# Kernel optimization log

Measured on AMD Instinct MI355X. Metric: run time of the kernel, lower is better.

## Reference

```python
import jax, jax.numpy as jnp
import numpy as np
from jax import lax

N, M, B = 512, 1024, 1024  # signal dim, atoms, batch (batch==m required by X = W @ Gamma)
POWER_ITER = 100
IHT_ITER = 50


def setup_inputs() -> dict:
    key = jax.random.key(0)
    k1, k2 = jax.random.split(key)
    Y = jax.random.normal(k1, (B, N), dtype=jnp.float32)
    W = jax.random.normal(k2, (N, M), dtype=jnp.float32)
    return {"Y": Y, "W": W, "K": 64}


def power_method(W):
    # 100 iterations of X <- X W^T W / ||.||; returns last pre-normalization norm
    # (approx largest eigenvalue of W^T W), matching PowerMethod in the source.
    X0 = jax.random.normal(jax.random.key(42), (1, W.shape[1]), dtype=W.dtype)

    def body(i, carry):
        X, _ = carry
        X2 = (X @ W.T) @ W          # [1, m]
        nm = jnp.linalg.norm(X2)
        return (X2 / nm, nm)

    _, nm = lax.fori_loop(0, POWER_ITER, body, (X0, jnp.asarray(1.0, W.dtype)))
    return nm


def hard_threshold_k(G, K):
    # keep entries strictly larger (in abs) than the (K+1)-th largest per row
    a = jnp.sort(jnp.abs(G), axis=1)[:, ::-1]   # descending per row
    T = a[:, K][:, None]                          # [B, 1]
    return G * (jnp.abs(G) > T).astype(G.dtype)


def reference(Y, W, K):
    # NormDict: column-normalize the dictionary
    W = W / jnp.linalg.norm(W, axis=0)
    c = power_method(W)
    eta = 1.0 / c
    Yn = jnp.linalg.norm(Y)

    # IHT sparse coding
    Gamma = hard_threshold_k(Y @ (eta * W), K)     # [B, m]
    residual = Gamma @ W.T - Y                      # [B, n]

    def step(carry, _):
        Gamma, residual = carry
        Gamma = hard_threshold_k(Gamma - eta * (residual @ W), K)
        residual = Gamma @ W.T - Y
        return (Gamma, residual), jnp.linalg.norm(residual) / Yn

    (Gamma, residual), norms = lax.scan(step, (Gamma, residual), None, length=IHT_ITER)

    X = W @ Gamma  # [n, m] @ [B, m] -> requires B == m, as in the torch source
    return X, Gamma, norms
```

## Files before the change

kernel.cpp:

```cpp
#include <hip/hip_runtime.h>


#define DEV __device__ __forceinline__

constexpr int Nd = 512;
constexpr int Md = 1024;
constexpr int Bd = 1024;
constexpr int Ksp = 64;
constexpr int IHT = 50;

DEV float wave_reduce_f(float v) {
#pragma unroll
  for (int off = 32; off > 0; off >>= 1) v += __shfl_down(v, off);
  return v;
}
DEV double wave_reduce_d(double v) {
#pragma unroll
  for (int off = 32; off > 0; off >>= 1) v += __shfl_down(v, off);
  return v;
}

__global__ void k_zero(double* dacc) {
  int t = threadIdx.x;
  if (t < 51) dacc[t] = 0.0;
}

__global__ __launch_bounds__(256) void k_colnorm(const float* __restrict__ W,
                                                 float* __restrict__ cnorm) {
  int col = blockIdx.x * 256 + threadIdx.x;
  double ss = 0.0;
  for (int i = 0; i < Nd; ++i) {
    float w = W[(size_t)i * Md + col];
    ss = fma((double)w, (double)w, ss);
  }
  cnorm[col] = (float)sqrt(ss);
}

__global__ __launch_bounds__(256) void k_normalize(const float* __restrict__ W,
                                                   const float* __restrict__ cnorm,
                                                   float* __restrict__ Wn) {
  int idx = blockIdx.x * 256 + threadIdx.x;
  Wn[idx] = W[idx] / cnorm[idx & (Md - 1)];
}

__global__ __launch_bounds__(256) void k_yn2(const float* __restrict__ Y,
                                             double* __restrict__ dacc) {
  double s = 0.0;
  for (int i = blockIdx.x * 256 + threadIdx.x; i < Bd * Nd; i += gridDim.x * 256) {
    float y = Y[i];
    s = fma((double)y, (double)y, s);
  }
  s = wave_reduce_d(s);
  __shared__ double red[4];
  int lane = threadIdx.x & 63, wid = threadIdx.x >> 6;
  if (lane == 0) red[wid] = s;
  __syncthreads();
  if (threadIdx.x == 0) atomicAdd(&dacc[0], red[0] + red[1] + red[2] + red[3]);
}

template <int BM, int BN, int TN>
__global__ __launch_bounds__(256) void k_gemm_t(const float* __restrict__ A, int lda, int ta,
                                                const float* __restrict__ B, int ldb, int tb,
                                                float* __restrict__ C, int ldc, int Kd,
                                                float scale) {
  constexpr int AE = 32 * BM / 256;
  constexpr int BE = 32 * BN / 256;
  __shared__ __align__(16) float As[32][BM + 4];
  __shared__ __align__(16) float Bs[32][BN + 4];
  const int tid = threadIdx.x;
  const int tx = tid % (BN / TN), ty = tid / (BN / TN);
  const int m0 = blockIdx.y * BM, n0 = blockIdx.x * BN;
  float ra[AE], rb[BE];
  float acc[4][TN];
#pragma unroll
  for (int i = 0; i < 4; ++i)
#pragma unroll
    for (int j = 0; j < TN; ++j) acc[i][j] = 0.f;

  auto loadA = [&](int k0) {
    if (!ta) {
      const int c = tid & 31, r0 = tid >> 5;
#pragma unroll
      for (int i = 0; i < AE; ++i)
        ra[i] = A[(size_t)(m0 + r0 + i * 8) * lda + (k0 + c)];
    } else {
      const int r = tid % BM, c0 = tid / BM;
#pragma unroll
      for (int i = 0; i < AE; ++i)
        ra[i] = A[(size_t)(k0 + c0 + i * (256 / BM)) * lda + (m0 + r)];
    }
  };
  auto storeA = [&]() {
    if (!ta) {
      const int c = tid & 31, r0 = tid >> 5;
#pragma unroll
      for (int i = 0; i < AE; ++i) As[c][r0 + i * 8] = ra[i];
    } else {
      const int r = tid % BM, c0 = tid / BM;
#pragma unroll
      for (int i = 0; i < AE; ++i) As[c0 + i * (256 / BM)][r] = ra[i];
    }
  };
  auto loadB = [&](int k0) {
    if (!tb) {
      const int c = tid % BN, r0 = tid / BN;
#pragma unroll
      for (int i = 0; i < BE; ++i)
        rb[i] = B[(size_t)(k0 + r0 + i * (256 / BN)) * ldb + (n0 + c)];
    } else {
      const int r = tid & 31, c0 = tid >> 5;
#pragma unroll
      for (int i = 0; i < BE; ++i)
        rb[i] = B[(size_t)(n0 + c0 + i * 8) * ldb + (k0 + r)];
    }
  };
  auto storeB = [&]() {
    if (!tb) {
      const int c = tid % BN, r0 = tid / BN;
#pragma unroll
      for (int i = 0; i < BE; ++i) Bs[r0 + i * (256 / BN)][c] = rb[i];
    } else {
      const int r = tid & 31, c0 = tid >> 5;
#pragma unroll
      for (int i = 0; i < BE; ++i) Bs[r][c0 + i * 8] = rb[i];
    }
  };

  loadA(0);
  loadB(0);
  storeA();
  storeB();
  __syncthreads();
  for (int k0 = 0; k0 < Kd; k0 += 32) {
    const bool more = (k0 + 32) < Kd;
    if (more) { loadA(k0 + 32); loadB(k0 + 32); }
#pragma unroll
    for (int kk = 0; kk < 32; ++kk) {
      const float4 a4 = *(const float4*)&As[kk][ty * 4];
      const float aa[4] = {a4.x, a4.y, a4.z, a4.w};
      float bb[TN];
      if constexpr (TN == 4) {
        const float4 b4 = *(const float4*)&Bs[kk][tx * 4];
        bb[0] = b4.x; bb[1] = b4.y; bb[2] = b4.z; bb[3] = b4.w;
      } else {
        const float2 b2 = *(const float2*)&Bs[kk][tx * 2];
        bb[0] = b2.x; bb[1] = b2.y;
      }
#pragma unroll
      for (int i = 0; i < 4; ++i)
#pragma unroll
        for (int j = 0; j < TN; ++j) acc[i][j] = fmaf(aa[i], bb[j], acc[i][j]);
    }
    if (more) {
      __syncthreads();
      storeA();
      storeB();
      __syncthreads();
    }
  }
#pragma unroll
  for (int i = 0; i < 4; ++i) {
    if constexpr (TN == 4) {
      float4 o;
      o.x = acc[i][0] * scale; o.y = acc[i][1] * scale;
      o.z = acc[i][2] * scale; o.w = acc[i][3] * scale;
      *(float4*)&C[(size_t)(m0 + ty * 4 + i) * ldc + n0 + tx * 4] = o;
    } else {
      float2 o;
      o.x = acc[i][0] * scale; o.y = acc[i][1] * scale;
      *(float2*)&C[(size_t)(m0 + ty * 4 + i) * ldc + n0 + tx * 2] = o;
    }
  }
}

DEV float erfinv_xla(float x) {
  float w = -log1pf(-x * x);
  float p;
  if (w < 5.0f) {
    w = w - 2.5f;
    p = 2.81022636e-08f;
    p = fmaf(p, w, 3.43273939e-07f);
    p = fmaf(p, w, -3.5233877e-06f);
    p = fmaf(p, w, -4.39150654e-06f);
    p = fmaf(p, w, 0.00021858087f);
    p = fmaf(p, w, -0.00125372503f);
    p = fmaf(p, w, -0.00417768164f);
    p = fmaf(p, w, 0.246640727f);
    p = fmaf(p, w, 1.50140941f);
  } else {
    w = sqrtf(w) - 3.0f;
    p = -0.000200214257f;
    p = fmaf(p, w, 0.000100950558f);
    p = fmaf(p, w, 0.00134934322f);
    p = fmaf(p, w, -0.00367342844f);
    p = fmaf(p, w, 0.00573950773f);
    p = fmaf(p, w, -0.0076224613f);
    p = fmaf(p, w, 0.00943887047f);
    p = fmaf(p, w, 1.00167406f);
    p = fmaf(p, w, 2.83297682f);
  }
  return p * x;
}

#define TF_ROUND(r)                                  \
  {                                                  \
    x0 += x1;                                        \
    x1 = (x1 << (r)) | (x1 >> (32 - (r)));           \
    x1 ^= x0;                                        \
  }

__global__ void k_x0(float* __restrict__ X0) {
  unsigned i = threadIdx.x;
  unsigned x0 = i, x1 = i + 512u;
  const unsigned ks0 = 0u, ks1 = 42u, ks2 = 0x1BD11BDAu ^ 42u;
  x0 += ks0; x1 += ks1;
  TF_ROUND(13) TF_ROUND(15) TF_ROUND(26) TF_ROUND(6)  x0 += ks1; x1 += ks2 + 1u;
  TF_ROUND(17) TF_ROUND(29) TF_ROUND(16) TF_ROUND(24) x0 += ks2; x1 += ks0 + 2u;
  TF_ROUND(13) TF_ROUND(15) TF_ROUND(26) TF_ROUND(6)  x0 += ks0; x1 += ks1 + 3u;
  TF_ROUND(17) TF_ROUND(29) TF_ROUND(16) TF_ROUND(24) x0 += ks1; x1 += ks2 + 4u;
  TF_ROUND(13) TF_ROUND(15) TF_ROUND(26) TF_ROUND(6)  x0 += ks2; x1 += ks0 + 5u;
  const float lo = -0.99999994f;
  const float sqrt2 = 1.41421356237f;
  {
    float f = __uint_as_float((x0 >> 9) | 0x3f800000u) - 1.0f;
    float u = fmaxf(lo, f * 2.0f + lo);
    X0[i] = sqrt2 * erfinv_xla(u);
  }
  {
    float f = __uint_as_float((x1 >> 9) | 0x3f800000u) - 1.0f;
    float u = fmaxf(lo, f * 2.0f + lo);
    X0[i + 512] = sqrt2 * erfinv_xla(u);
  }
}

__global__ __launch_bounds__(256) void k_z0(const float* __restrict__ X0,
                                            const float* __restrict__ Wn,
                                            float* __restrict__ vout) {
  const int lane = threadIdx.x & 63, wid = threadIdx.x >> 6;
  const int row = blockIdx.x * 4 + wid;
  const float4* wr = (const float4*)(Wn + (size_t)row * Md);
  const float4* x4 = (const float4*)X0;
  float s = 0.f;
#pragma unroll
  for (int e = 0; e < 4; ++e) {
    const float4 w4 = wr[lane + e * 64];
    const float4 xx = x4[lane + e * 64];
    s = fmaf(w4.x, xx.x, s); s = fmaf(w4.y, xx.y, s);
    s = fmaf(w4.z, xx.z, s); s = fmaf(w4.w, xx.w, s);
  }
  s = wave_reduce_f(s);
  if (lane == 0) vout[row] = s;
}

__global__ __launch_bounds__(256) void k_pmv(const float* __restrict__ Mmat,
                                             const float* __restrict__ vin,
                                             float* __restrict__ vout, float scale) {
  const int lane = threadIdx.x & 63, wid = threadIdx.x >> 6;
  const int row = blockIdx.x * 4 + wid;
  const float4* mr = (const float4*)(Mmat + (size_t)row * Nd);
  const float4* v4 = (const float4*)vin;
  float s = 0.f;
#pragma unroll
  for (int e = 0; e < 2; ++e) {
    const float4 m4 = mr[lane + e * 64];
    const float4 xx = v4[lane + e * 64];
    s = fmaf(m4.x, xx.x, s); s = fmaf(m4.y, xx.y, s);
    s = fmaf(m4.z, xx.z, s); s = fmaf(m4.w, xx.w, s);
  }
  s = wave_reduce_f(s);
  if (lane == 0) vout[row] = s * scale;
}

__global__ __launch_bounds__(512) void k_pfinal(const float* __restrict__ v99,
                                                const float* __restrict__ v100,
                                                float* __restrict__ cbuf) {
  __shared__ double r99[8], r100[8];
  const int t = threadIdx.x, lane = t & 63, wid = t >> 6;
  double a = (double)v99[t]; a *= a;
  double b = (double)v100[t]; b *= b;
  a = wave_reduce_d(a);
  b = wave_reduce_d(b);
  if (lane == 0) { r99[wid] = a; r100[wid] = b; }
  __syncthreads();
  if (t == 0) {
    double n99 = 0.0, n100 = 0.0;
    for (int i = 0; i < 8; ++i) { n99 += r99[i]; n100 += r100[i]; }
    float c = (float)(8.0 * sqrt(n100 / n99));
    cbuf[0] = c;
    cbuf[1] = 1.0f / c;
  }
}

__global__ __launch_bounds__(256) void k_iht_all(
    const float* __restrict__ Q, const float* __restrict__ YW,
    const float* __restrict__ cbuf, float* __restrict__ gdense,
    double* __restrict__ normacc) {
  __shared__ float u[Md];
  __shared__ float sval[Ksp];
  __shared__ int sidx[Ksp];
  __shared__ unsigned hist[256];
  __shared__ unsigned wred[4];
  __shared__ unsigned sel_need, sel_prefix;
  __shared__ double dred[4];
  __shared__ int scnt;

  const int t = threadIdx.x;
  const int b = blockIdx.x;
  const int lane = t & 63, wv = t >> 6;
  const float eta = cbuf[1];
  const float4 yw = ((const float4*)(YW + (size_t)b * Md))[t];
  const float4* Q4 = (const float4*)Q;

  for (int it = -1; it < IHT; ++it) {
    if (it >= 0) {
      const int cnt = scnt;
      float4 p = make_float4(0.f, 0.f, 0.f, 0.f);
      int k = 0;
      for (; k + 4 <= cnt; k += 4) {
        const int i0 = sidx[k], i1 = sidx[k + 1], i2 = sidx[k + 2], i3 = sidx[k + 3];
        const float g0 = sval[k], g1 = sval[k + 1], g2 = sval[k + 2], g3 = sval[k + 3];
        const float4 q0 = Q4[(size_t)i0 * 256 + t];
        const float4 q1 = Q4[(size_t)i1 * 256 + t];
        const float4 q2 = Q4[(size_t)i2 * 256 + t];
        const float4 q3 = Q4[(size_t)i3 * 256 + t];
        p.x = fmaf(g0, q0.x, p.x); p.x = fmaf(g1, q1.x, p.x);
        p.x = fmaf(g2, q2.x, p.x); p.x = fmaf(g3, q3.x, p.x);
        p.y = fmaf(g0, q0.y, p.y); p.y = fmaf(g1, q1.y, p.y);
        p.y = fmaf(g2, q2.y, p.y); p.y = fmaf(g3, q3.y, p.y);
        p.z = fmaf(g0, q0.z, p.z); p.z = fmaf(g1, q1.z, p.z);
        p.z = fmaf(g2, q2.z, p.z); p.z = fmaf(g3, q3.z, p.z);
        p.w = fmaf(g0, q0.w, p.w); p.w = fmaf(g1, q1.w, p.w);
        p.w = fmaf(g2, q2.w, p.w); p.w = fmaf(g3, q3.w, p.w);
      }
      for (; k < cnt; ++k) {
        const int id = sidx[k];
        const float g = sval[k];
        const float4 q = Q4[(size_t)id * 256 + t];
        p.x = fmaf(g, q.x, p.x); p.y = fmaf(g, q.y, p.y);
        p.z = fmaf(g, q.z, p.z); p.w = fmaf(g, q.w, p.w);
      }
      ((float4*)u)[t] = p;
      __syncthreads();
      if (it >= 1) {
        double part = 0.0;
        if (t < cnt) {
          const int id = sidx[t];
          part = (double)sval[t] * ((double)u[id] - 2.0 * (double)YW[(size_t)b * Md + id]);
        }
        part = wave_reduce_d(part);
        if (lane == 0) dred[wv] = part;
        __syncthreads();
        if (t == 0) atomicAdd(&normacc[it - 1], dred[0] + dred[1] + dred[2] + dred[3]);
        __syncthreads();
      }
      float4 uu;
      uu.x = -(eta * (p.x - yw.x)); uu.y = -(eta * (p.y - yw.y));
      uu.z = -(eta * (p.z - yw.z)); uu.w = -(eta * (p.w - yw.w));
      ((float4*)u)[t] = uu;
      __syncthreads();
      if (t < cnt) u[sidx[t]] += sval[t];
      __syncthreads();
    } else {
      float4 uu;
      uu.x = eta * yw.x; uu.y = eta * yw.y; uu.z = eta * yw.z; uu.w = eta * yw.w;
      ((float4*)u)[t] = uu;
      __syncthreads();
    }

    float vals[4];
    unsigned key[4];
    {
      const float4 mv = ((const float4*)u)[t];
      vals[0] = mv.x; vals[1] = mv.y; vals[2] = mv.z; vals[3] = mv.w;
#pragma unroll
      for (int e = 0; e < 4; ++e) key[e] = __float_as_uint(vals[e]) & 0x7fffffffu;
    }

    unsigned need = Ksp + 1, prefix = 0u, pmask = 0u;
    for (int pass = 3; pass >= 0; --pass) {
      const int sh = 8 * pass;
      hist[t] = 0u;
      __syncthreads();
#pragma unroll
      for (int e = 0; e < 4; ++e)
        if ((key[e] & pmask) == prefix) atomicAdd(&hist[(key[e] >> sh) & 255u], 1u);
      __syncthreads();
      const unsigned h = hist[t];
      unsigned x = h;
#pragma unroll
      for (int off = 1; off < 64; off <<= 1) {
        const unsigned y = __shfl_down(x, off);
        if (lane + off < 64) x += y;
      }
      if (lane == 0) wred[wv] = x;
      __syncthreads();
      unsigned addhi = 0u;
      for (int w2 = wv + 1; w2 < 4; ++w2) addhi += wred[w2];
      const unsigned incl = x + addhi;
      const unsigned excl = incl - h;
      if (incl >= need && excl < need) {
        sel_prefix = prefix | ((unsigned)t << sh);
        sel_need = need - excl;
      }
      __syncthreads();
      prefix = sel_prefix;
      need = sel_need;
      pmask |= (255u << sh);
    }
    const unsigned Tbits = prefix;

    unsigned keep = 0u;
    unsigned myc = 0u;
#pragma unroll
    for (int e = 0; e < 4; ++e)
      if (key[e] > Tbits) { keep |= (1u << e); ++myc; }
    unsigned x = myc;
#pragma unroll
    for (int off = 1; off < 64; off <<= 1) {
      const unsigned y = __shfl_up(x, off);
      if (lane >= off) x += y;
    }
    __syncthreads();
    if (lane == 63) wred[wv] = x;
    __syncthreads();
    unsigned addlo = 0u;
    for (int w2 = 0; w2 < wv; ++w2) addlo += wred[w2];
    int base = (int)(x + addlo) - (int)myc;
#pragma unroll
    for (int e = 0; e < 4; ++e) {
      if (keep & (1u << e)) {
        sidx[base] = t * 4 + e;
        sval[base] = vals[e];
        ++base;
      }
    }
    if (t == 0) scnt = (int)(wred[0] + wred[1] + wred[2] + wred[3]);
    if (it == IHT - 1) {
      float4 g;
      g.x = (keep & 1u) ? vals[0] : 0.f;
      g.y = (keep & 2u) ? vals[1] : 0.f;
      g.z = (keep & 4u) ? vals[2] : 0.f;
      g.w = (keep & 8u) ? vals[3] : 0.f;
      ((float4*)(gdense + (size_t)b * Md))[t] = g;
    }
    __syncthreads();
  }

  const int cnt = scnt;
  if (wv == 0) {
    double part = 0.0;
    if (lane < cnt) {
      const int id = sidx[lane];
      float acc2 = 0.f;
      for (int k = 0; k < cnt; ++k)
        acc2 = fmaf(sval[k], Q[(size_t)sidx[k] * Md + id], acc2);
      part = (double)sval[lane] * ((double)acc2 - 2.0 * (double)YW[(size_t)b * Md + id]);
    }
    part = wave_reduce_d(part);
    if (lane == 0) atomicAdd(&normacc[IHT - 1], part);
  }
}

__global__ void k_wnorms(const double* __restrict__ dacc, float* __restrict__ onorms) {
  const int t = threadIdx.x;
  if (t < IHT) {
    const double yn2 = dacc[0];
    double r2 = yn2 + dacc[1 + t];
    if (r2 < 0.0) r2 = 0.0;
    onorms[t] = (float)(sqrt(r2) / sqrt(yn2));
  }
}

extern "C" void kernel_launch(void* const* d_in, const int* in_sizes, int n_in,
                              void* d_out, int out_size, void* d_ws, size_t ws_size,
                              hipStream_t stream) {
  (void)in_sizes; (void)n_in; (void)out_size; (void)ws_size;
  const float* Y = (const float*)d_in[0];
  const float* W = (const float*)d_in[1];
  float* out = (float*)d_out;
  float* outX = out;
  float* outG = out + Nd * Md;
  float* outN = outG + Bd * Md;

  char* wsb = (char*)d_ws;
  double* dacc = (double*)wsb;
  float* cbuf = (float*)(wsb + 512);
  float* Wn = (float*)(wsb + 1024);
  float* Q = Wn + Nd * Md;
  float* YW = Q + Md * Md;
  float* Smat = YW + Bd * Md;
  float* S2 = Smat + Nd * Nd;
  float* cnorm = S2 + Nd * Nd;
  float* X0 = cnorm + Md;
  float* V = X0 + Md;

  k_zero<<<1, 64, 0, stream>>>(dacc);
  k_colnorm<<<4, 256, 0, stream>>>(W, cnorm);
  k_normalize<<<2048, 256, 0, stream>>>(W, cnorm, Wn);

  k_gemm_t<64, 32, 2><<<dim3(16, 8), 256, 0, stream>>>(Wn, Md, 0, Wn, Md, 1, Smat, Nd, Md, 1.0f);
  k_gemm_t<64, 32, 2><<<dim3(16, 8), 256, 0, stream>>>(Smat, Nd, 0, Smat, Nd, 0, S2, Nd, Nd, 0.015625f);
  k_gemm_t<64, 64, 4><<<dim3(16, 16), 256, 0, stream>>>(Wn, Md, 1, Wn, Md, 0, Q, Md, Nd, 1.0f);
  k_gemm_t<64, 64, 4><<<dim3(16, 16), 256, 0, stream>>>(Y, Nd, 0, Wn, Md, 0, YW, Md, Nd, 1.0f);
  k_yn2<<<128, 256, 0, stream>>>(Y, dacc);

  k_x0<<<1, 512, 0, stream>>>(X0);
  k_z0<<<128, 256, 0, stream>>>(X0, Wn, V);
  float* pin = V;
  float* pout = V + 512;
  for (int i = 0; i < 49; ++i) {
    k_pmv<<<128, 256, 0, stream>>>(S2, pin, pout, 1.0f);
    float* tp = pin; pin = pout; pout = tp;
  }
  k_pmv<<<128, 256, 0, stream>>>(Smat, pin, V + 1024, 0.125f);
  k_pmv<<<128, 256, 0, stream>>>(Smat, V + 1024, V + 1536, 0.125f);
  k_pfinal<<<1, 512, 0, stream>>>(V + 1024, V + 1536, cbuf);

  k_iht_all<<<1024, 256, 0, stream>>>(Q, YW, cbuf, outG, dacc + 1);
  k_wnorms<<<1, 64, 0, stream>>>(dacc, outN);

  k_gemm_t<64, 32, 2><<<dim3(32, 8), 256, 0, stream>>>(Wn, Md, 0, outG, Md, 0, outX, Md, Md, 1.0f);
}
```

Before: 1.093 ms.

## Cut barriers in IHT radix-select with per-wave double-buffered histograms

Reworks the per-row IHT kernel's radix select so that each wave writes its own histogram, using double buffering. This removes the zeroing barrier, and a single wave then merges the histograms and scans four bins per lane. The gather loop is unrolled to 8 rows, and the sparse indices and values are made uniform via readfirstlane so they can use scalar registers. The YW row is cached in LDS for the norm term, and a few barriers are merged or removed. The aim is to cut synchronisation and latency in the 50-iteration serial loop, at the cost of more LDS per block and some serial work on wave 0.

```diff
diff --git a/kernel.cpp b/kernel.cpp
--- a/kernel.cpp
+++ b/kernel.cpp
@@ -18,6 +18,9 @@
 #pragma unroll
   for (int off = 32; off > 0; off >>= 1) v += __shfl_down(v, off);
   return v;
+}
+DEV float rfl_f(float v) {
+  return __uint_as_float(__builtin_amdgcn_readfirstlane(__float_as_uint(v)));
 }
 
 __global__ void k_zero(double* dacc) {
@@ -296,9 +299,10 @@
     const float* __restrict__ cbuf, float* __restrict__ gdense,
     double* __restrict__ normacc) {
   __shared__ float u[Md];
+  __shared__ float yws[Md];
   __shared__ float sval[Ksp];
   __shared__ int sidx[Ksp];
-  __shared__ unsigned hist[256];
+  __shared__ unsigned histbuf[2][4][256];
   __shared__ unsigned wred[4];
   __shared__ unsigned sel_need, sel_prefix;
   __shared__ double dred[4];
@@ -309,33 +313,44 @@
   const int lane = t & 63, wv = t >> 6;
   const float eta = cbuf[1];
   const float4 yw = ((const float4*)(YW + (size_t)b * Md))[t];
-  const float4* Q4 = (const float4*)Q;
+  ((float4*)yws)[t] = yw;
+#pragma unroll
+  for (int e = 0; e < 8; ++e) ((unsigned*)histbuf)[t + e * 256] = 0u;
+  const float* Qt = Q + t * 4;
 
   for (int it = -1; it < IHT; ++it) {
     if (it >= 0) {
       const int cnt = scnt;
       float4 p = make_float4(0.f, 0.f, 0.f, 0.f);
       int k = 0;
-      for (; k + 4 <= cnt; k += 4) {
-        const int i0 = sidx[k], i1 = sidx[k + 1], i2 = sidx[k + 2], i3 = sidx[k + 3];
-        const float g0 = sval[k], g1 = sval[k + 1], g2 = sval[k + 2], g3 = sval[k + 3];
-        const float4 q0 = Q4[(size_t)i0 * 256 + t];
-        const float4 q1 = Q4[(size_t)i1 * 256 + t];
-        const float4 q2 = Q4[(size_t)i2 * 256 + t];
-        const float4 q3 = Q4[(size_t)i3 * 256 + t];
+      for (; k + 8 <= cnt; k += 8) {
+#define GROW(j)                                                        \
+        const int id##j = __builtin_amdgcn_readfirstlane(sidx[k + j]); \
+        const float g##j = rfl_f(sval[k + j]);                         \
+        const float4 q##j = *(const float4*)(Qt + (size_t)id##j * Md);
+        GROW(0) GROW(1) GROW(2) GROW(3) GROW(4) GROW(5) GROW(6) GROW(7)
+#undef GROW
         p.x = fmaf(g0, q0.x, p.x); p.x = fmaf(g1, q1.x, p.x);
         p.x = fmaf(g2, q2.x, p.x); p.x = fmaf(g3, q3.x, p.x);
+        p.x = fmaf(g4, q4.x, p.x); p.x = fmaf(g5, q5.x, p.x);
+        p.x = fmaf(g6, q6.x, p.x); p.x = fmaf(g7, q7.x, p.x);
         p.y = fmaf(g0, q0.y, p.y); p.y = fmaf(g1, q1.y, p.y);
         p.y = fmaf(g2, q2.y, p.y); p.y = fmaf(g3, q3.y, p.y);
+        p.y = fmaf(g4, q4.y, p.y); p.y = fmaf(g5, q5.y, p.y);
+        p.y = fmaf(g6, q6.y, p.y); p.y = fmaf(g7, q7.y, p.y);
         p.z = fmaf(g0, q0.z, p.z); p.z = fmaf(g1, q1.z, p.z);
         p.z = fmaf(g2, q2.z, p.z); p.z = fmaf(g3, q3.z, p.z);
+        p.z = fmaf(g4, q4.z, p.z); p.z = fmaf(g5, q5.z, p.z);
+        p.z = fmaf(g6, q6.z, p.z); p.z = fmaf(g7, q7.z, p.z);
         p.w = fmaf(g0, q0.w, p.w); p.w = fmaf(g1, q1.w, p.w);
         p.w = fmaf(g2, q2.w, p.w); p.w = fmaf(g3, q3.w, p.w);
+        p.w = fmaf(g4, q4.w, p.w); p.w = fmaf(g5, q5.w, p.w);
+        p.w = fmaf(g6, q6.w, p.w); p.w = fmaf(g7, q7.w, p.w);
       }
       for (; k < cnt; ++k) {
-        const int id = sidx[k];
-        const float g = sval[k];
-        const float4 q = Q4[(size_t)id * 256 + t];
+        const int id = __builtin_amdgcn_readfirstlane(sidx[k]);
+        const float g = rfl_f(sval[k]);
+        const float4 q = *(const float4*)(Qt + (size_t)id * Md);
         p.x = fmaf(g, q.x, p.x); p.y = fmaf(g, q.y, p.y);
         p.z = fmaf(g, q.z, p.z); p.w = fmaf(g, q.w, p.w);
       }
@@ -345,14 +360,14 @@
         double part = 0.0;
         if (t < cnt) {
           const int id = sidx[t];
-          part = (double)sval[t] * ((double)u[id] - 2.0 * (double)YW[(size_t)b * Md + id]);
+          part = (double)sval[t] * ((double)u[id] - 2.0 * (double)yws[id]);
         }
         part = wave_reduce_d(part);
         if (lane == 0) dred[wv] = part;
-        __syncthreads();
-        if (t == 0) atomicAdd(&normacc[it - 1], dred[0] + dred[1] + dred[2] + dred[3]);
-        __syncthreads();
       }
+      __syncthreads();
+      if (it >= 1 && t == 0)
+        atomicAdd(&normacc[it - 1], dred[0] + dred[1] + dred[2] + dred[3]);
       float4 uu;
       uu.x = -(eta * (p.x - yw.x)); uu.y = -(eta * (p.y - yw.y));
       uu.z = -(eta * (p.z - yw.z)); uu.w = -(eta * (p.w - yw.w));
@@ -377,30 +392,40 @@
     }
 
     unsigned need = Ksp + 1, prefix = 0u, pmask = 0u;
+#pragma unroll
     for (int pass = 3; pass >= 0; --pass) {
       const int sh = 8 * pass;
-      hist[t] = 0u;
-      __syncthreads();
+      const int pb = pass & 1;
+      unsigned(*hist)[256] = histbuf[pb];
 #pragma unroll
       for (int e = 0; e < 4; ++e)
-        if ((key[e] & pmask) == prefix) atomicAdd(&hist[(key[e] >> sh) & 255u], 1u);
-      __syncthreads();
-      const unsigned h = hist[t];
-      unsigned x = h;
-#pragma unroll
-      for (int off = 1; off < 64; off <<= 1) {
-        const unsigned y = __shfl_down(x, off);
-        if (lane + off < 64) x += y;
-      }
-      if (lane == 0) wred[wv] = x;
-      __syncthreads();
-      unsigned addhi = 0u;
-      for (int w2 = wv + 1; w2 < 4; ++w2) addhi += wred[w2];
-      const unsigned incl = x + addhi;
-      const unsigned excl = incl - h;
-      if (incl >= need && excl < need) {
-        sel_prefix = prefix | ((unsigned)t << sh);
-        sel_need = need - excl;
+        if ((key[e] & pmask) == prefix) atomicAdd(&hist[wv][(key[e] >> sh) & 255u], 1u);
+      __syncthreads();
+      unsigned* hz = histbuf[pb ^ 1][wv];
+      hz[lane] = 0u; hz[lane + 64] = 0u; hz[lane + 128] = 0u; hz[lane + 192] = 0u;
+      if (wv == 0) {
+        const unsigned c0 = hist[0][lane] + hist[1][lane] + hist[2][lane] + hist[3][lane];
+        const unsigned c1 = hist[0][lane + 64] + hist[1][lane + 64] + hist[2][lane + 64] + hist[3][lane + 64];
+        const unsigned c2 = hist[0][lane + 128] + hist[1][lane + 128] + hist[2][lane + 128] + hist[3][lane + 128];
+        const unsigned c3 = hist[0][lane + 192] + hist[1][lane + 192] + hist[2][lane + 192] + hist[3][lane + 192];
+        unsigned s0 = c0, s1 = c1, s2 = c2, s3 = c3;
+#pragma unroll
+        for (int off = 1; off < 64; off <<= 1) {
+          const unsigned y0 = __shfl_down(s0, off), y1 = __shfl_down(s1, off);
+          const unsigned y2 = __shfl_down(s2, off), y3 = __shfl_down(s3, off);
+          if (lane + off < 64) { s0 += y0; s1 += y1; s2 += y2; s3 += y3; }
+        }
+        const unsigned T1 = __builtin_amdgcn_readfirstlane(s1);
+        const unsigned T2 = __builtin_amdgcn_readfirstlane(s2);
+        const unsigned T3 = __builtin_amdgcn_readfirstlane(s3);
+        const unsigned i0 = s0 + T1 + T2 + T3;
+        const unsigned i1 = s1 + T2 + T3;
+        const unsigned i2 = s2 + T3;
+        const unsigned i3 = s3;
+        if (i0 >= need && i0 - c0 < need) { sel_prefix = prefix | ((unsigned)lane << sh); sel_need = need - (i0 - c0); }
+        if (i1 >= need && i1 - c1 < need) { sel_prefix = prefix | ((unsigned)(lane + 64) << sh); sel_need = need - (i1 - c1); }
+        if (i2 >= need && i2 - c2 < need) { sel_prefix = prefix | ((unsigned)(lane + 128) << sh); sel_need = need - (i2 - c2); }
+        if (i3 >= need && i3 - c3 < need) { sel_prefix = prefix | ((unsigned)(lane + 192) << sh); sel_need = need - (i3 - c3); }
       }
       __syncthreads();
       prefix = sel_prefix;
@@ -420,7 +445,6 @@
       const unsigned y = __shfl_up(x, off);
       if (lane >= off) x += y;
     }
-    __syncthreads();
     if (lane == 63) wred[wv] = x;
     __syncthreads();
     unsigned addlo = 0u;
@@ -454,7 +478,7 @@
       float acc2 = 0.f;
       for (int k = 0; k < cnt; ++k)
         acc2 = fmaf(sval[k], Q[(size_t)sidx[k] * Md + id], acc2);
-      part = (double)sval[lane] * ((double)acc2 - 2.0 * (double)YW[(size_t)b * Md + id]);
+      part = (double)sval[lane] * ((double)acc2 - 2.0 * (double)yws[id]);
     }
     part = wave_reduce_d(part);
     if (lane == 0) atomicAdd(&normacc[IHT - 1], part);
```

Measured after the change: 978.2 us. 10.5% less time.
